# Performance work log

Hardware: AMD Instinct MI355X
Metric: run time of the kernel (lower is better)

The kernel has to match this reference:

```python
import jax, jax.numpy as jnp
import numpy as np

K = 7  # local_kernel_size


def conv2d(x, w, b, pad):
    # x: [B,C,H,W], w: [O,I,kh,kw]
    y = jax.lax.conv_general_dilated(
        x, w, window_strides=(1, 1), padding=[(pad, pad), (pad, pad)],
        dimension_numbers=("NCHW", "OIHW", "NCHW"))
    return y + b[None, :, None, None]


def kernel_normalize(kernel, k):
    # kernel: [B, k*k, H, W]; zero-mean over tap dim, then add 1/(k*k)
    km = jnp.mean(kernel, axis=1, keepdims=True)
    return kernel - km + 1.0 / (k * k)


def local_conv_feat(img, kernel, k):
    # Fused dynamic local conv: avoids materializing [B,C,k*k,H,W].
    # Tap order matches F.unfold row-major (dy, dx).
    B, C, H, W = img.shape
    pad = (k - 1) // 2
    imgp = jnp.pad(img, ((0, 0), (0, 0), (pad, pad), (pad, pad)))
    out = jnp.zeros_like(img)
    for dy in range(k):
        for dx in range(k):
            idx = dy * k + dx
            out = out + imgp[:, :, dy:dy + H, dx:dx + W] * kernel[:, idx:idx + 1]
    return out


def setup_inputs() -> dict:
    key = jax.random.key(0)
    ks = jax.random.split(key, 14)
    B, C, H, W = 4, 64, 128, 128
    w = lambda k, shape: jax.random.normal(k, shape, jnp.float32) * 0.05
    return {
        "x": jax.random.normal(ks[0], (B, C, H, W), jnp.float32),
        "kernel_features": jax.random.normal(ks[1], (B, C, H, W), jnp.float32),
        # feature_path: two 3x3 convs
        "fw1": w(ks[2], (C, C, 3, 3)), "fb1": jnp.zeros((C,), jnp.float32),
        "fw2": w(ks[3], (C, C, 3, 3)), "fb2": jnp.zeros((C,), jnp.float32),
        # multiplicative_path: two 3x3 convs
        "mw1": w(ks[4], (C, C, 3, 3)), "mb1": jnp.zeros((C,), jnp.float32),
        "mw2": w(ks[5], (C, C, 3, 3)), "mb2": jnp.zeros((C,), jnp.float32),
        # local_filter_path: two 1x1 convs, last outputs k*k channels
        "lw1": w(ks[6], (C, C, 1, 1)), "lb1": jnp.zeros((C,), jnp.float32),
        "lw2": w(ks[7], (K * K, C, 1, 1)), "lb2": jnp.zeros((K * K,), jnp.float32),
    }


def reference(x, kernel_features, fw1, fb1, fw2, fb2, mw1, mb1, mw2, mb2, lw1, lb1, lw2, lb2):
    # feature_path: ReLU -> conv3x3 -> ReLU -> conv3x3
    fp = conv2d(jax.nn.relu(conv2d(jax.nn.relu(x), fw1, fb1, 1)), fw2, fb2, 1)
    # multiplicative_path: conv3x3 -> ReLU -> conv3x3
    mp = conv2d(jax.nn.relu(conv2d(kernel_features, mw1, mb1, 1)), mw2, mb2, 1)
    # local_filter_path: conv1x1 -> ReLU -> conv1x1 (-> k*k channels)
    lp = conv2d(jax.nn.relu(conv2d(kernel_features, lw1, lb1, 0)), lw2, lb2, 0)
    lp = kernel_normalize(lp, K)
    feat = fp * mp
    filtered = local_conv_feat(feat, lp, K)
    return x + filtered
```

## Files before the change

### kernel.cpp

```cpp
#include <hip/hip_runtime.h>
#include <hip/hip_bf16.h>

#define Cc 64
#define Hc 128
#define Wc 128
#define HWc (Hc * Wc)
#define Bc 4

typedef __attribute__((ext_vector_type(8))) short short8;
typedef __attribute__((ext_vector_type(4))) float float4v;

static __device__ __forceinline__ unsigned short f2bu(float f) {
    __hip_bfloat16 h = __float2bfloat16(f);
    return *(unsigned short*)&h;
}

static __device__ __forceinline__ void gl_lds16(const void* g, void* l) {
    __builtin_amdgcn_global_load_lds(
        (const __attribute__((address_space(1))) unsigned int*)g,
        (__attribute__((address_space(3))) unsigned int*)l, 16, 0, 0);
}

__global__ __launch_bounds__(256) void prep_k(
    const float* __restrict__ x, const float* __restrict__ kf,
    const float* __restrict__ fw1, const float* __restrict__ fw2,
    const float* __restrict__ mw1, const float* __restrict__ mw2,
    const float* __restrict__ lw1, const float* __restrict__ lw2,
    unsigned short* __restrict__ xb, unsigned short* __restrict__ kfb,
    unsigned short* __restrict__ wbase)
{
    const int bid = blockIdx.x;
    const int tid = threadIdx.x;

    if (bid < 512) {
        const bool isx = bid < 256;
        const float* src = isx ? x : kf;
        unsigned short* dst = isx ? xb : kfb;
        const int px = (isx ? bid : bid - 256) * 256 + tid;
        const int b  = px >> 14;
        const int hw = px & 16383;
        const float* s = src + (size_t)b * Cc * HWc + hw;
        unsigned short* d = dst + (size_t)px * Cc;
#pragma unroll
        for (int c8 = 0; c8 < 8; ++c8) {
            unsigned int pk[4];
#pragma unroll
            for (int jp = 0; jp < 4; ++jp) {
                float v0 = s[(size_t)(c8 * 8 + jp * 2 + 0) * HWc];
                float v1 = s[(size_t)(c8 * 8 + jp * 2 + 1) * HWc];
                if (isx) { v0 = fmaxf(v0, 0.f); v1 = fmaxf(v1, 0.f); }
                pk[jp] = (unsigned int)f2bu(v0) | ((unsigned int)f2bu(v1) << 16);
            }
            *(uint4*)(d + c8 * 8) = make_uint4(pk[0], pk[1], pk[2], pk[3]);
        }
    } else if (bid < 584) {
        const int wbid  = bid - 512;
        const int which = wbid / 18;
        const float* w = (which == 0) ? fw1 : (which == 1) ? fw2 : (which == 2) ? mw1 : mw2;
        unsigned short* wb = wbase + (size_t)which * 36864;
        const int g = (wbid % 18) * 256 + tid;
        if (g >= 4608) return;
        const int lane = g & 63;
        const int smt  = g >> 6;
        const int s    = smt >> 2;
        const int mt   = smt & 3;
        const int co   = mt * 16 + (lane & 15);
        const int kb   = s * 32 + (lane >> 4) * 8;
        unsigned int pk[4];
#pragma unroll
        for (int jp = 0; jp < 4; ++jp) {
            int k0 = kb + jp * 2, k1 = k0 + 1;
            float v0 = w[((size_t)co * Cc + (k0 & 63)) * 9 + (k0 >> 6)];
            float v1 = w[((size_t)co * Cc + (k1 & 63)) * 9 + (k1 >> 6)];
            pk[jp] = (unsigned int)f2bu(v0) | ((unsigned int)f2bu(v1) << 16);
        }
        *(uint4*)(wb + (size_t)g * 8) = make_uint4(pk[0], pk[1], pk[2], pk[3]);
    } else {
        const int wbid  = bid - 584;
        const int which = wbid >> 1;
        const float* w = which ? lw2 : lw1;
        const int Cout = which ? 49 : 64;
        unsigned short* wb = wbase + 4 * 36864 + (size_t)which * 4096;
        const int g = (wbid & 1) * 256 + tid;
        const int lane = g & 63;
        const int smt  = g >> 6;
        const int s    = smt >> 2;
        const int mt   = smt & 3;
        const int co   = mt * 16 + (lane & 15);
        const int kb   = s * 32 + (lane >> 4) * 8;
        unsigned int pk[4];
#pragma unroll
        for (int jp = 0; jp < 4; ++jp) {
            int k0 = kb + jp * 2, k1 = k0 + 1;
            float v0 = (co < Cout) ? w[(size_t)co * Cc + k0] : 0.f;
            float v1 = (co < Cout) ? w[(size_t)co * Cc + k1] : 0.f;
            pk[jp] = (unsigned int)f2bu(v0) | ((unsigned int)f2bu(v1) << 16);
        }
        *(uint4*)(wb + (size_t)g * 8) = make_uint4(pk[0], pk[1], pk[2], pk[3]);
    }
}

#define STAGE_DMA(INPTR, SBUF)                                                \
    for (int k = wv; k < 33; k += 4) {                                        \
        const int u_  = k * 8 + (lane >> 3);                                  \
        const int j_  = lane & 7;                                             \
        const int r_  = u_ / 66;                                              \
        const int c_  = u_ - r_ * 66;                                         \
        const int gh_ = h0 - 1 + r_;                                          \
        const int gw_ = w0 - 1 + c_;                                          \
        const bool ok_ = ((unsigned)gh_ < (unsigned)Hc) && ((unsigned)gw_ < (unsigned)Wc); \
        const int ch_ = j_ ^ (u_ & 7);                                        \
        const unsigned short* g_ = ok_                                        \
            ? (INPTR) + ((((size_t)b * Hc + gh_) * Wc + gw_) << 6) + (ch_ << 3) \
            : zpage + (ch_ << 3);                                             \
        gl_lds16(g_, &(SBUF)[k * 512]);                                       \
    }

#define LOAD_A(W, s, m) (*(const short8*)((W) + (size_t)(s) * 2048 + (size_t)(m) * 512))
#define LOAD_B(SB, s, nt) ({                                                  \
        const int tap_ = (s) >> 1;                                            \
        const int qb_  = rowb[tap_ / 3] + tap_ % 3;                           \
        const int ch0_ = ((s) & 1) * 4 + quad;                                \
        *(const short8*)&(SB)[(qb_ + (nt) * 16) * 64 + ((ch0_ ^ (qb_ & 7)) << 3)]; })

#define CONV_GEMM(APTR, ACC, SB)                                              \
    {                                                                         \
        short8 a_buf[4][2], b_cur[4], b_nxt[4];                               \
        _Pragma("unroll")                                                     \
        for (int q = 0; q < 3; ++q)                                           \
            _Pragma("unroll")                                                 \
            for (int m = 0; m < 2; ++m) a_buf[q][m] = LOAD_A(APTR, q, m);     \
        _Pragma("unroll")                                                     \
        for (int nt = 0; nt < 4; ++nt) b_cur[nt] = LOAD_B(SB, 0, nt);         \
        _Pragma("unroll")                                                     \
        for (int s = 0; s < 18; ++s) {                                        \
            if (s + 3 < 18) {                                                 \
                _Pragma("unroll")                                             \
                for (int m = 0; m < 2; ++m)                                   \
                    a_buf[(s + 3) & 3][m] = LOAD_A(APTR, s + 3, m);           \
            }                                                                 \
            if (s + 1 < 18) {                                                 \
                _Pragma("unroll")                                             \
                for (int nt = 0; nt < 4; ++nt)                                \
                    b_nxt[nt] = LOAD_B(SB, s + 1, nt);                        \
            }                                                                 \
            _Pragma("unroll")                                                 \
            for (int nt = 0; nt < 4; ++nt)                                    \
                _Pragma("unroll")                                             \
                for (int m = 0; m < 2; ++m)                                   \
                    ACC[m][nt] = __builtin_amdgcn_mfma_f32_16x16x32_bf16(     \
                        a_buf[s & 3][m], b_cur[nt], ACC[m][nt], 0, 0, 0);     \
            if (s + 1 < 18) {                                                 \
                _Pragma("unroll")                                             \
                for (int nt = 0; nt < 4; ++nt) b_cur[nt] = b_nxt[nt];         \
            }                                                                 \
        }                                                                     \
    }

__global__ __launch_bounds__(256) void conv1_lp_k(
    const unsigned short* __restrict__ in0,
    const unsigned short* __restrict__ in1,
    const unsigned short* __restrict__ wfrag0,
    const unsigned short* __restrict__ wfrag1,
    const float* __restrict__ bias0,
    const float* __restrict__ bias1,
    const unsigned short* __restrict__ zpage,
    unsigned short* __restrict__ out0,
    unsigned short* __restrict__ out1,
    const unsigned short* __restrict__ w1, const float* __restrict__ b1,
    const unsigned short* __restrict__ w2, const float* __restrict__ b2,
    float* __restrict__ lpout)
{
    __shared__ unsigned short s_b[264 * 64];

    const int tid  = threadIdx.x;
    const int lane = tid & 63;
    const int wv   = tid >> 6;
    const int quad = lane >> 4;
    const int zz   = blockIdx.z;

    if (zz < 8) {
        const int w0   = blockIdx.x * 64;
        const int h0   = blockIdx.y * 2;
        const int b    = zz & 3;
        const bool sel = zz >> 2;

        const unsigned short* in    = sel ? in1 : in0;
        const unsigned short* wfrag = sel ? wfrag1 : wfrag0;
        const float*          bias  = sel ? bias1 : bias0;
        unsigned short*       out   = sel ? out1 : out0;

        STAGE_DMA(in, s_b);
        __syncthreads();

        const int rowsel = wv >> 1;
        const int cohalf = wv & 1;
        const int n15    = lane & 15;
        const unsigned short* aptr = wfrag + (((size_t)(cohalf * 2) * 64 + lane) << 3);

        int rowb[3];
#pragma unroll
        for (int ky = 0; ky < 3; ++ky) rowb[ky] = (rowsel + ky) * 66 + n15;

        float4v acc[2][4];
#pragma unroll
        for (int m = 0; m < 2; ++m)
#pragma unroll
            for (int nt = 0; nt < 4; ++nt) acc[m][nt] = (float4v){0.f, 0.f, 0.f, 0.f};

        CONV_GEMM(aptr, acc, s_b);

        const int h = h0 + rowsel;
#pragma unroll
        for (int m = 0; m < 2; ++m) {
            const int mt  = cohalf * 2 + m;
            const int co0 = mt * 16 + quad * 4;
            float4 bv = *(const float4*)&bias[co0];
#pragma unroll
            for (int nt = 0; nt < 4; ++nt) {
                const size_t pix = ((size_t)b * Hc + h) * Wc + w0 + nt * 16 + n15;
                ushort4 pk;
                pk.x = f2bu(fmaxf(acc[m][nt][0] + bv.x, 0.f));
                pk.y = f2bu(fmaxf(acc[m][nt][1] + bv.y, 0.f));
                pk.z = f2bu(fmaxf(acc[m][nt][2] + bv.z, 0.f));
                pk.w = f2bu(fmaxf(acc[m][nt][3] + bv.w, 0.f));
                *(ushort4*)&out[pix * Cc + co0] = pk;
            }
        }
    } else {
        const int lpid = (zz - 8) * 128 + blockIdx.y * 2 + blockIdx.x;
        const int p    = lane & 15;
        const size_t pix = (size_t)lpid * 64 + wv * 16 + p;
        unsigned short* st = &s_b[wv * 1024];

        float4v acc1[4];
#pragma unroll
        for (int mt = 0; mt < 4; ++mt) acc1[mt] = (float4v){0.f, 0.f, 0.f, 0.f};
#pragma unroll
        for (int s = 0; s < 2; ++s) {
            short8 bfr = *(const short8*)&in1[pix * Cc + s * 32 + quad * 8];
#pragma unroll
            for (int mt = 0; mt < 4; ++mt) {
                short8 afr = *(const short8*)&w1[(size_t)(((s * 4 + mt) << 6) + lane) << 3];
                acc1[mt] = __builtin_amdgcn_mfma_f32_16x16x32_bf16(afr, bfr, acc1[mt], 0, 0, 0);
            }
        }

#pragma unroll
        for (int mt = 0; mt < 4; ++mt) {
            const int co0 = mt * 16 + quad * 4;
            float4 bv = *(const float4*)&b1[co0];
            ushort4 pk;
            pk.x = f2bu(fmaxf(acc1[mt][0] + bv.x, 0.f));
            pk.y = f2bu(fmaxf(acc1[mt][1] + bv.y, 0.f));
            pk.z = f2bu(fmaxf(acc1[mt][2] + bv.z, 0.f));
            pk.w = f2bu(fmaxf(acc1[mt][3] + bv.w, 0.f));
            const int cg = co0 >> 3;
            *(ushort4*)&st[p * 64 + ((cg ^ (p & 7)) << 3) + (quad & 1) * 4] = pk;
        }
        __syncthreads();

        float4v acc2[4];
#pragma unroll
        for (int mt = 0; mt < 4; ++mt) acc2[mt] = (float4v){0.f, 0.f, 0.f, 0.f};
#pragma unroll
        for (int s = 0; s < 2; ++s) {
            const int cg = s * 4 + quad;
            short8 bfr = *(const short8*)&st[p * 64 + ((cg ^ (p & 7)) << 3)];
#pragma unroll
            for (int mt = 0; mt < 4; ++mt) {
                short8 afr = *(const short8*)&w2[(size_t)(((s * 4 + mt) << 6) + lane) << 3];
                acc2[mt] = __builtin_amdgcn_mfma_f32_16x16x32_bf16(afr, bfr, acc2[mt], 0, 0, 0);
            }
        }

        float v[4][4];
        float partial = 0.f;
#pragma unroll
        for (int mt = 0; mt < 4; ++mt) {
#pragma unroll
            for (int r = 0; r < 4; ++r) {
                const int tap = mt * 16 + quad * 4 + r;
                float val = (tap < 49) ? (acc2[mt][r] + b2[tap]) : 0.f;
                v[mt][r] = val;
                partial += val;
            }
        }
        partial += __shfl_xor(partial, 16, 64);
        partial += __shfl_xor(partial, 32, 64);
        const float m = partial * (1.f / 49.f) - (1.f / 49.f);

        const int b  = (int)(pix >> 14);
        const int hw = (int)(pix & 16383);
#pragma unroll
        for (int mt = 0; mt < 4; ++mt) {
#pragma unroll
            for (int r = 0; r < 4; ++r) {
                const int tap = mt * 16 + quad * 4 + r;
                if (tap < 49)
                    lpout[((size_t)b * 49 + tap) * HWc + hw] = v[mt][r] - m;
            }
        }
    }
}

__global__ __launch_bounds__(256) void conv2_fused_k(
    const unsigned short* __restrict__ t1f,
    const unsigned short* __restrict__ t1m,
    const unsigned short* __restrict__ wf,
    const unsigned short* __restrict__ wm,
    const float* __restrict__ bf,
    const float* __restrict__ bm,
    const unsigned short* __restrict__ zpage,
    float* __restrict__ feat)
{
    __shared__ unsigned short s_b2[2][264 * 64];

    const int tid  = threadIdx.x;
    const int lane = tid & 63;
    const int wv   = tid >> 6;
    const int w0   = blockIdx.x * 64;
    const int h0   = blockIdx.y * 2;
    const int b    = blockIdx.z;

    STAGE_DMA(t1f, s_b2[0]);
    STAGE_DMA(t1m, s_b2[1]);
    __syncthreads();

    const int rowsel = wv >> 1;
    const int cohalf = wv & 1;
    const int quad   = lane >> 4;
    const int n15    = lane & 15;

    int rowb[3];
#pragma unroll
    for (int ky = 0; ky < 3; ++ky) rowb[ky] = (rowsel + ky) * 66 + n15;

    float4v acc[2][4];
#pragma unroll
    for (int m = 0; m < 2; ++m)
#pragma unroll
        for (int nt = 0; nt < 4; ++nt) acc[m][nt] = (float4v){0.f, 0.f, 0.f, 0.f};

    {
        const unsigned short* aptr = wf + (((size_t)(cohalf * 2) * 64 + lane) << 3);
        CONV_GEMM(aptr, acc, s_b2[0]);
    }

    unsigned int fpk[2][4][2];
#pragma unroll
    for (int m = 0; m < 2; ++m) {
        const int mt  = cohalf * 2 + m;
        const int co0 = mt * 16 + quad * 4;
        float4 bv = *(const float4*)&bf[co0];
#pragma unroll
        for (int nt = 0; nt < 4; ++nt) {
            fpk[m][nt][0] = (unsigned int)f2bu(acc[m][nt][0] + bv.x)
                          | ((unsigned int)f2bu(acc[m][nt][1] + bv.y) << 16);
            fpk[m][nt][1] = (unsigned int)f2bu(acc[m][nt][2] + bv.z)
                          | ((unsigned int)f2bu(acc[m][nt][3] + bv.w) << 16);
        }
    }

#pragma unroll
    for (int m = 0; m < 2; ++m)
#pragma unroll
        for (int nt = 0; nt < 4; ++nt) acc[m][nt] = (float4v){0.f, 0.f, 0.f, 0.f};

    {
        const unsigned short* aptr = wm + (((size_t)(cohalf * 2) * 64 + lane) << 3);
        CONV_GEMM(aptr, acc, s_b2[1]);
    }

    const int h = h0 + rowsel;
#pragma unroll
    for (int m = 0; m < 2; ++m) {
        const int mt  = cohalf * 2 + m;
        const int co0 = mt * 16 + quad * 4;
        float4 bv = *(const float4*)&bm[co0];
#pragma unroll
        for (int nt = 0; nt < 4; ++nt) {
            float v[4] = {acc[m][nt][0] + bv.x, acc[m][nt][1] + bv.y,
                          acc[m][nt][2] + bv.z, acc[m][nt][3] + bv.w};
            v[0] *= __uint_as_float((fpk[m][nt][0] & 0xffffu) << 16);
            v[1] *= __uint_as_float(fpk[m][nt][0] & 0xffff0000u);
            v[2] *= __uint_as_float((fpk[m][nt][1] & 0xffffu) << 16);
            v[3] *= __uint_as_float(fpk[m][nt][1] & 0xffff0000u);
#pragma unroll
            for (int r = 0; r < 4; ++r)
                feat[((size_t)b * Cc + co0 + r) * HWc + (size_t)h * Wc + w0 + nt * 16 + n15] = v[r];
        }
    }
}

__global__ __launch_bounds__(256) void local_conv_v2(
    const float* __restrict__ x, const float* __restrict__ feat,
    const float* __restrict__ lp, float* __restrict__ out)
{
    const int tid = threadIdx.x;
    const int w4  = (tid & 31) * 4;
    const int ro  = tid >> 5;
    const int h   = blockIdx.y * 8 + ro;
    const int c0  = blockIdx.x * 4;
    const int b   = blockIdx.z;

    float msk[12];
#pragma unroll
    for (int e = 0; e < 12; ++e) {
        int gw = w4 - 4 + e;
        msk[e] = ((unsigned)gw < (unsigned)Wc) ? 1.f : 0.f;
    }

    float acc[4][4];
#pragma unroll
    for (int ch = 0; ch < 4; ++ch)
#pragma unroll
        for (int p = 0; p < 4; ++p) acc[ch][p] = 0.f;

    const float* lpb = lp + (size_t)b * 49 * HWc + (size_t)h * Wc + w4;
    const float* fb  = feat + ((size_t)b * Cc + c0) * HWc;

#pragma unroll
    for (int dy = 0; dy < 7; ++dy) {
        const int gh = h + dy - 3;
        if ((unsigned)gh >= (unsigned)Hc) continue;

        float4 lp4[7];
#pragma unroll
        for (int dx = 0; dx < 7; ++dx)
            lp4[dx] = *(const float4*)&lpb[(size_t)(dy * 7 + dx) * HWc];

        const float* frow = fb + (size_t)gh * Wc + w4;
#pragma unroll
        for (int ch = 0; ch < 4; ++ch) {
            const float* fr = frow + (size_t)ch * HWc;
            float4 a  = *(const float4*)(fr - 4);
            float4 bq = *(const float4*)(fr);
            float4 cq = *(const float4*)(fr + 4);
            float f[12];
            f[0]  = a.x;            f[1]  = a.y * msk[1];
            f[2]  = a.z * msk[2];   f[3]  = a.w * msk[3];
            f[4]  = bq.x;           f[5]  = bq.y;
            f[6]  = bq.z;           f[7]  = bq.w;
            f[8]  = cq.x * msk[8];  f[9]  = cq.y * msk[9];
            f[10] = cq.z * msk[10]; f[11] = cq.w;
#pragma unroll
            for (int dx = 0; dx < 7; ++dx) {
                const float* lpv = (const float*)&lp4[dx];
#pragma unroll
                for (int p = 0; p < 4; ++p)
                    acc[ch][p] = fmaf(f[p + dx + 1], lpv[p], acc[ch][p]);
            }
        }
    }

#pragma unroll
    for (int ch = 0; ch < 4; ++ch) {
        const size_t idx = ((size_t)b * Cc + c0 + ch) * HWc + (size_t)h * Wc + w4;
        float4 xv = *(const float4*)&x[idx];
        float4 r  = {acc[ch][0] + xv.x, acc[ch][1] + xv.y,
                     acc[ch][2] + xv.z, acc[ch][3] + xv.w};
        *(float4*)&out[idx] = r;
    }
}

extern "C" void kernel_launch(void* const* d_in, const int* in_sizes, int n_in,
                              void* d_out, int out_size, void* d_ws, size_t ws_size,
                              hipStream_t stream)
{
    const float* x   = (const float*)d_in[0];
    const float* kf  = (const float*)d_in[1];
    const float* fw1 = (const float*)d_in[2];
    const float* fb1 = (const float*)d_in[3];
    const float* fw2 = (const float*)d_in[4];
    const float* fb2 = (const float*)d_in[5];
    const float* mw1 = (const float*)d_in[6];
    const float* mb1 = (const float*)d_in[7];
    const float* mw2 = (const float*)d_in[8];
    const float* mb2 = (const float*)d_in[9];
    const float* lw1 = (const float*)d_in[10];
    const float* lb1 = (const float*)d_in[11];
    const float* lw2 = (const float*)d_in[12];
    const float* lb2 = (const float*)d_in[13];

    float* out = (float*)d_out;
    char*  ws  = (char*)d_ws;

    const size_t NBH = (size_t)Bc * HWc * Cc * 2;
    const size_t NBF = (size_t)Bc * Cc * HWc * 4;
    const size_t LPB = (size_t)Bc * 49 * HWc * 4;
    const size_t WBA = (size_t)(4 * 36864 + 2 * 4096) * 2;

    unsigned short* t1f   = (unsigned short*)(ws);
    unsigned short* t1m   = (unsigned short*)(ws + NBH);
    float*          feat  = (float*)(ws + 2 * NBH);
    float*          lpb   = (float*)(ws + 2 * NBH + NBF);
    unsigned short* xb    = (unsigned short*)(ws + 2 * NBH + NBF + LPB);
    unsigned short* kfb   = (unsigned short*)((char*)xb + NBH);
    unsigned short* wbase = (unsigned short*)((char*)kfb + NBH);
    unsigned short* zpage = (unsigned short*)((char*)wbase + WBA);
    unsigned short* wb1   = wbase;
    unsigned short* wb2   = wbase + 36864;
    unsigned short* wb3   = wbase + 2 * 36864;
    unsigned short* wb4   = wbase + 3 * 36864;
    unsigned short* wl1   = wbase + 4 * 36864;
    unsigned short* wl2   = wbase + 4 * 36864 + 4096;

    dim3 blk(256);
    dim3 gc1(Wc / 64, Hc / 2, 16);
    dim3 gm (Wc / 64, Hc / 2, Bc);
    dim3 glc(Cc / 4, Hc / 8, Bc);

    hipMemsetAsync(zpage, 0, 256, stream);

    prep_k<<<dim3(588), blk, 0, stream>>>(x, kf, fw1, fw2, mw1, mw2, lw1, lw2,
                                          xb, kfb, wbase);

    conv1_lp_k<<<gc1, blk, 0, stream>>>(xb, kfb, wb1, wb3, fb1, mb1, zpage,
                                        t1f, t1m, wl1, lb1, wl2, lb2, lpb);

    conv2_fused_k<<<gm, blk, 0, stream>>>(t1f, t1m, wb2, wb4, fb2, mb2, zpage, feat);

    local_conv_v2<<<glc, blk, 0, stream>>>(x, feat, lpb, out);
}
```

Before: 178.6 us.

## Store feat and local filter intermediates in bf16 with channel-last feat layout

The product features are now written as bf16 in an NHWC layout, and the normalized local filter taps are written as bf16. The local conv kernel reads packed bf16 values (four channels per 8-byte load) and unpacks them to fp32 for the FMAs. This cuts the intermediate traffic written and read between kernels roughly in half, at the cost of bf16 rounding of feat and the filter weights. The NHWC writes and reads use 8-byte accesses strided by 64 channels, so coalescing changes.

```diff
diff --git a/kernel.cpp b/kernel.cpp
--- a/kernel.cpp
+++ b/kernel.cpp
@@ -13,6 +13,12 @@
 static __device__ __forceinline__ unsigned short f2bu(float f) {
     __hip_bfloat16 h = __float2bfloat16(f);
     return *(unsigned short*)&h;
+}
+static __device__ __forceinline__ float bulo(unsigned int u) {
+    return __uint_as_float((u & 0xffffu) << 16);
+}
+static __device__ __forceinline__ float buhi(unsigned int u) {
+    return __uint_as_float(u & 0xffff0000u);
 }
 
 static __device__ __forceinline__ void gl_lds16(const void* g, void* l) {
@@ -169,7 +175,7 @@
     unsigned short* __restrict__ out1,
     const unsigned short* __restrict__ w1, const float* __restrict__ b1,
     const unsigned short* __restrict__ w2, const float* __restrict__ b2,
-    float* __restrict__ lpout)
+    unsigned short* __restrict__ lpout)
 {
     __shared__ unsigned short s_b[264 * 64];
 
@@ -298,7 +304,7 @@
             for (int r = 0; r < 4; ++r) {
                 const int tap = mt * 16 + quad * 4 + r;
                 if (tap < 49)
-                    lpout[((size_t)b * 49 + tap) * HWc + hw] = v[mt][r] - m;
+                    lpout[((size_t)b * 49 + tap) * HWc + hw] = f2bu(v[mt][r] - m);
             }
         }
     }
@@ -312,7 +318,7 @@
     const float* __restrict__ bf,
     const float* __restrict__ bm,
     const unsigned short* __restrict__ zpage,
-    float* __restrict__ feat)
+    unsigned short* __restrict__ featb)
 {
     __shared__ unsigned short s_b2[2][264 * 64];
 
@@ -347,7 +353,7 @@
         CONV_GEMM(aptr, acc, s_b2[0]);
     }
 
-    unsigned int fpk[2][4][2];
+    float fpv[2][4][4];
 #pragma unroll
     for (int m = 0; m < 2; ++m) {
         const int mt  = cohalf * 2 + m;
@@ -355,10 +361,10 @@
         float4 bv = *(const float4*)&bf[co0];
 #pragma unroll
         for (int nt = 0; nt < 4; ++nt) {
-            fpk[m][nt][0] = (unsigned int)f2bu(acc[m][nt][0] + bv.x)
-                          | ((unsigned int)f2bu(acc[m][nt][1] + bv.y) << 16);
-            fpk[m][nt][1] = (unsigned int)f2bu(acc[m][nt][2] + bv.z)
-                          | ((unsigned int)f2bu(acc[m][nt][3] + bv.w) << 16);
+            fpv[m][nt][0] = bulo((unsigned int)f2bu(acc[m][nt][0] + bv.x));
+            fpv[m][nt][1] = bulo((unsigned int)f2bu(acc[m][nt][1] + bv.y));
+            fpv[m][nt][2] = bulo((unsigned int)f2bu(acc[m][nt][2] + bv.z));
+            fpv[m][nt][3] = bulo((unsigned int)f2bu(acc[m][nt][3] + bv.w));
         }
     }
 
@@ -380,22 +386,20 @@
         float4 bv = *(const float4*)&bm[co0];
 #pragma unroll
         for (int nt = 0; nt < 4; ++nt) {
-            float v[4] = {acc[m][nt][0] + bv.x, acc[m][nt][1] + bv.y,
-                          acc[m][nt][2] + bv.z, acc[m][nt][3] + bv.w};
-            v[0] *= __uint_as_float((fpk[m][nt][0] & 0xffffu) << 16);
-            v[1] *= __uint_as_float(fpk[m][nt][0] & 0xffff0000u);
-            v[2] *= __uint_as_float((fpk[m][nt][1] & 0xffffu) << 16);
-            v[3] *= __uint_as_float(fpk[m][nt][1] & 0xffff0000u);
-#pragma unroll
-            for (int r = 0; r < 4; ++r)
-                feat[((size_t)b * Cc + co0 + r) * HWc + (size_t)h * Wc + w0 + nt * 16 + n15] = v[r];
-        }
-    }
-}
-
-__global__ __launch_bounds__(256) void local_conv_v2(
-    const float* __restrict__ x, const float* __restrict__ feat,
-    const float* __restrict__ lp, float* __restrict__ out)
+            const size_t pix = ((size_t)b * Hc + h) * Wc + w0 + nt * 16 + n15;
+            ushort4 pk;
+            pk.x = f2bu((acc[m][nt][0] + bv.x) * fpv[m][nt][0]);
+            pk.y = f2bu((acc[m][nt][1] + bv.y) * fpv[m][nt][1]);
+            pk.z = f2bu((acc[m][nt][2] + bv.z) * fpv[m][nt][2]);
+            pk.w = f2bu((acc[m][nt][3] + bv.w) * fpv[m][nt][3]);
+            *(ushort4*)&featb[pix * Cc + co0] = pk;
+        }
+    }
+}
+
+__global__ __launch_bounds__(256) void local_conv_v3(
+    const float* __restrict__ x, const unsigned short* __restrict__ featb,
+    const unsigned short* __restrict__ lp, float* __restrict__ out)
 {
     const int tid = threadIdx.x;
     const int w4  = (tid & 31) * 4;
@@ -404,11 +408,11 @@
     const int c0  = blockIdx.x * 4;
     const int b   = blockIdx.z;
 
-    float msk[12];
-#pragma unroll
-    for (int e = 0; e < 12; ++e) {
+    float msk[11];
+#pragma unroll
+    for (int e = 1; e <= 10; ++e) {
         int gw = w4 - 4 + e;
-        msk[e] = ((unsigned)gw < (unsigned)Wc) ? 1.f : 0.f;
+        msk[e - 1] = ((unsigned)gw < (unsigned)Wc) ? 1.f : 0.f;
     }
 
     float acc[4][4];
@@ -417,40 +421,41 @@
 #pragma unroll
         for (int p = 0; p < 4; ++p) acc[ch][p] = 0.f;
 
-    const float* lpb = lp + (size_t)b * 49 * HWc + (size_t)h * Wc + w4;
-    const float* fb  = feat + ((size_t)b * Cc + c0) * HWc;
+    const unsigned short* lpb = lp + (size_t)b * 49 * HWc + (size_t)h * Wc + w4;
+    const unsigned short* fbb = featb + ((size_t)b * Hc) * Wc * Cc + c0;
 
 #pragma unroll
     for (int dy = 0; dy < 7; ++dy) {
         const int gh = h + dy - 3;
         if ((unsigned)gh >= (unsigned)Hc) continue;
 
-        float4 lp4[7];
-#pragma unroll
-        for (int dx = 0; dx < 7; ++dx)
-            lp4[dx] = *(const float4*)&lpb[(size_t)(dy * 7 + dx) * HWc];
-
-        const float* frow = fb + (size_t)gh * Wc + w4;
+        float lpf[7][4];
+#pragma unroll
+        for (int dx = 0; dx < 7; ++dx) {
+            uint2 lv = *(const uint2*)&lpb[(size_t)(dy * 7 + dx) * HWc];
+            lpf[dx][0] = bulo(lv.x); lpf[dx][1] = buhi(lv.x);
+            lpf[dx][2] = bulo(lv.y); lpf[dx][3] = buhi(lv.y);
+        }
+
+        const unsigned short* frow = fbb + ((size_t)gh * Wc + w4 - 4) * Cc;
+        uint2 fraw[10];
+#pragma unroll
+        for (int e = 1; e <= 10; ++e)
+            fraw[e - 1] = *(const uint2*)&frow[(size_t)e * Cc];
+
 #pragma unroll
         for (int ch = 0; ch < 4; ++ch) {
-            const float* fr = frow + (size_t)ch * HWc;
-            float4 a  = *(const float4*)(fr - 4);
-            float4 bq = *(const float4*)(fr);
-            float4 cq = *(const float4*)(fr + 4);
-            float f[12];
-            f[0]  = a.x;            f[1]  = a.y * msk[1];
-            f[2]  = a.z * msk[2];   f[3]  = a.w * msk[3];
-            f[4]  = bq.x;           f[5]  = bq.y;
-            f[6]  = bq.z;           f[7]  = bq.w;
-            f[8]  = cq.x * msk[8];  f[9]  = cq.y * msk[9];
-            f[10] = cq.z * msk[10]; f[11] = cq.w;
-#pragma unroll
-            for (int dx = 0; dx < 7; ++dx) {
-                const float* lpv = (const float*)&lp4[dx];
+            float f[10];
+#pragma unroll
+            for (int e = 0; e < 10; ++e) {
+                unsigned int raw = (ch < 2) ? fraw[e].x : fraw[e].y;
+                f[e] = ((ch & 1) ? buhi(raw) : bulo(raw)) * msk[e];
+            }
+#pragma unroll
+            for (int dx = 0; dx < 7; ++dx)
 #pragma unroll
                 for (int p = 0; p < 4; ++p)
-                    acc[ch][p] = fmaf(f[p + dx + 1], lpv[p], acc[ch][p]);
-            }
+                    acc[ch][p] = fmaf(f[p + dx], lpf[dx][p], acc[ch][p]);
         }
     }
 
@@ -487,15 +492,14 @@
     char*  ws  = (char*)d_ws;
 
     const size_t NBH = (size_t)Bc * HWc * Cc * 2;
-    const size_t NBF = (size_t)Bc * Cc * HWc * 4;
-    const size_t LPB = (size_t)Bc * 49 * HWc * 4;
+    const size_t LPH = (size_t)Bc * 49 * HWc * 2;
     const size_t WBA = (size_t)(4 * 36864 + 2 * 4096) * 2;
 
     unsigned short* t1f   = (unsigned short*)(ws);
     unsigned short* t1m   = (unsigned short*)(ws + NBH);
-    float*          feat  = (float*)(ws + 2 * NBH);
-    float*          lpb   = (float*)(ws + 2 * NBH + NBF);
-    unsigned short* xb    = (unsigned short*)(ws + 2 * NBH + NBF + LPB);
+    unsigned short* featb = (unsigned short*)(ws + 2 * NBH);
+    unsigned short* lpb   = (unsigned short*)(ws + 3 * NBH);
+    unsigned short* xb    = (unsigned short*)(ws + 3 * NBH + LPH);
     unsigned short* kfb   = (unsigned short*)((char*)xb + NBH);
     unsigned short* wbase = (unsigned short*)((char*)kfb + NBH);
     unsigned short* zpage = (unsigned short*)((char*)wbase + WBA);
@@ -519,7 +523,7 @@
     conv1_lp_k<<<gc1, blk, 0, stream>>>(xb, kfb, wb1, wb3, fb1, mb1, zpage,
                                         t1f, t1m, wl1, lb1, wl2, lb2, lpb);
 
-    conv2_fused_k<<<gm, blk, 0, stream>>>(t1f, t1m, wb2, wb4, fb2, mb2, zpage, feat);
-
-    local_conv_v2<<<glc, blk, 0, stream>>>(x, feat, lpb, out);
-}
+    conv2_fused_k<<<gm, blk, 0, stream>>>(t1f, t1m, wb2, wb4, fb2, mb2, zpage, featb);
+
+    local_conv_v3<<<glc, blk, 0, stream>>>(x, featb, lpb, out);
+}
```

Measured after the change: 231.3 us. 1.29x slower.
